# Optimization experiments

Hardware: AMD Instinct MI355X
Metric: run time of the kernel (lower is better)

Reference implementation:

```python
import jax, jax.numpy as jnp
import numpy as np

N_THRESHOLDS = 10


def setup_inputs() -> dict:
    key = jax.random.key(0)
    k1, k2, k3 = jax.random.split(key, 3)
    shape = (32, 1024, 1024)
    prediction = jax.random.normal(k1, shape, dtype=jnp.float32)
    mask = jax.random.randint(k2, shape, 0, 2, dtype=jnp.int32)
    target = jax.random.randint(k3, shape, 0, 2, dtype=jnp.int32)
    return {"prediction": prediction, "mask": mask, "target": target}


def reference(prediction, mask, target):
    # thresholds = linspace(0,1,n+2)[1:-1], same as the torch module
    thresholds = jnp.linspace(0.0, 1.0, N_THRESHOLDS + 2, dtype=jnp.float32)[1:-1]

    s = jax.nn.sigmoid(prediction).ravel()            # [N]
    m = mask.ravel().astype(bool)                     # [N] valid mask
    t = target.ravel().astype(bool)                   # [N]
    mt = m & t                                        # masked positives

    # Broadcast compare against all thresholds at once (single fused pass,
    # no per-threshold host sync like the original loop).
    pos = s[None, :] > thresholds[:, None]            # [T, N] bool

    tp = jnp.sum(pos & mt[None, :], axis=1)           # [T] int32
    p = jnp.sum(pos & m[None, :], axis=1)             # predicted-positive count

    total_m = jnp.sum(m)                              # total valid elements
    total_t = jnp.sum(mt)                             # total true positives in mask

    fp = p - tp
    fn = total_t - tp
    tn = total_m - p - fn

    # classes layout matches torch module: rows = [tp, fp, tn, fn]
    return jnp.stack([tp, fp, tn, fn], axis=0).astype(jnp.float32)
```

## Files before the change

### kernel.cpp

```cpp
#include <hip/hip_runtime.h>


#define NTHR 10
#define NBKT 11
#define NCNT 22
#define WS_STRIDE 16

typedef unsigned long long u64;

__device__ __forceinline__ unsigned wave_reduce_add(unsigned v) {
#pragma unroll
    for (int off = 32; off > 0; off >>= 1)
        v += __shfl_down(v, off, 64);
    return v;
}

__global__ __launch_bounds__(64) void zero_ws_kernel(unsigned* __restrict__ ws) {
    int i = threadIdx.x;
    if (i < NCNT) ws[i * WS_STRIDE] = 0u;
}

__device__ __forceinline__ void acc_elem(float pv, unsigned mm, unsigned tt,
                                         u64& hP, u64& hT) {
    const float L[NTHR] = {-2.3025851f, -1.5040774f, -0.98082925f, -0.55961579f,
                           -0.18232156f, 0.18232156f,  0.55961579f,  0.98082925f,
                            1.5040774f,  2.3025851f};
    unsigned mt = mm & tt;
    unsigned b = 0u;
#pragma unroll
    for (int j = 0; j < NTHR; ++j) b += (pv > L[j]) ? 1u : 0u;
    unsigned sh = (b << 2) + b;
    hP += (u64)mm << sh;
    hT += (u64)mt << sh;
}

__device__ __forceinline__ void acc_vec(const float4& p, const int4& m, const int4& t,
                                        u64& hP, u64& hT) {
    acc_elem(p.x, (unsigned)m.x, (unsigned)t.x, hP, hT);
    acc_elem(p.y, (unsigned)m.y, (unsigned)t.y, hP, hT);
    acc_elem(p.z, (unsigned)m.z, (unsigned)t.z, hP, hT);
    acc_elem(p.w, (unsigned)m.w, (unsigned)t.w, hP, hT);
}

__device__ __forceinline__ void flush_hist(u64& hP, u64& hT,
                                           u64& Plo, u64& Phi, u64& Tlo, u64& Thi) {
#pragma unroll
    for (int b = 0; b < 6; ++b) {
        Plo += (u64)((unsigned)(hP >> (5 * b)) & 31u) << (10 * b);
        Tlo += (u64)((unsigned)(hT >> (5 * b)) & 31u) << (10 * b);
    }
#pragma unroll
    for (int b = 6; b < NBKT; ++b) {
        Phi += (u64)((unsigned)(hP >> (5 * b)) & 31u) << (10 * (b - 6));
        Thi += (u64)((unsigned)(hT >> (5 * b)) & 31u) << (10 * (b - 6));
    }
    hP = 0ull; hT = 0ull;
}

__global__ __launch_bounds__(256, 2) void count_kernel(
        const float4* __restrict__ pred4,
        const int4*  __restrict__ mask4,
        const int4*  __restrict__ targ4,
        const float* __restrict__ pred,
        const int*   __restrict__ mask,
        const int*   __restrict__ targ,
        unsigned* __restrict__ ws, int nvec, int n) {
    u64 Plo = 0ull, Phi = 0ull, Tlo = 0ull, Thi = 0ull;

    const int tid    = blockIdx.x * blockDim.x + threadIdx.x;
    const int lane   = tid & 63;
    const int waveId = tid >> 6;
    const int totalWaves = (gridDim.x * blockDim.x) >> 6;
    const int strideG    = totalWaves << 8;

    float4 cp0, cp1, cp2, cp3;
    int4   cm0, cm1, cm2, cm3, ct0, ct1, ct2, ct3;

    int  base = waveId << 8;
    bool full = (base + 256 <= nvec);
    if (full) {
        cp0 = pred4[base +       lane]; cp1 = pred4[base +  64 + lane];
        cp2 = pred4[base + 128 + lane]; cp3 = pred4[base + 192 + lane];
        cm0 = mask4[base +       lane]; cm1 = mask4[base +  64 + lane];
        cm2 = mask4[base + 128 + lane]; cm3 = mask4[base + 192 + lane];
        ct0 = targ4[base +       lane]; ct1 = targ4[base +  64 + lane];
        ct2 = targ4[base + 128 + lane]; ct3 = targ4[base + 192 + lane];
    }

    while (base < nvec) {
        const int nb    = base + strideG;
        const bool nfull = (nb + 256 <= nvec);

        float4 np0, np1, np2, np3;
        int4   nm0, nm1, nm2, nm3, nt0, nt1, nt2, nt3;
        if (nfull) {
            np0 = pred4[nb +       lane]; np1 = pred4[nb +  64 + lane];
            np2 = pred4[nb + 128 + lane]; np3 = pred4[nb + 192 + lane];
            nm0 = mask4[nb +       lane]; nm1 = mask4[nb +  64 + lane];
            nm2 = mask4[nb + 128 + lane]; nm3 = mask4[nb + 192 + lane];
            nt0 = targ4[nb +       lane]; nt1 = targ4[nb +  64 + lane];
            nt2 = targ4[nb + 128 + lane]; nt3 = targ4[nb + 192 + lane];
        }

        u64 hP = 0ull, hT = 0ull;
        if (full) {
            acc_vec(cp0, cm0, ct0, hP, hT);
            acc_vec(cp1, cm1, ct1, hP, hT);
            acc_vec(cp2, cm2, ct2, hP, hT);
            acc_vec(cp3, cm3, ct3, hP, hT);
        } else {
#pragma unroll
            for (int c = 0; c < 4; ++c) {
                int g = base + (c << 6) + lane;
                if (g < nvec)
                    acc_vec(pred4[g], mask4[g], targ4[g], hP, hT);
            }
        }
        flush_hist(hP, hT, Plo, Phi, Tlo, Thi);

        cp0 = np0; cp1 = np1; cp2 = np2; cp3 = np3;
        cm0 = nm0; cm1 = nm1; cm2 = nm2; cm3 = nm3;
        ct0 = nt0; ct1 = nt1; ct2 = nt2; ct3 = nt3;
        full = nfull;
        base = nb;
    }

    {
        int i = nvec * 4 + tid;
        if (i < n) {
            u64 hP = 0ull, hT = 0ull;
            acc_elem(pred[i], (unsigned)mask[i], (unsigned)targ[i], hP, hT);
            flush_hist(hP, hT, Plo, Phi, Tlo, Thi);
        }
    }

    unsigned vals[NCNT];
#pragma unroll
    for (int b = 0; b < 6; ++b) {
        vals[b]        = (unsigned)(Plo >> (10 * b)) & 1023u;
        vals[NBKT + b] = (unsigned)(Tlo >> (10 * b)) & 1023u;
    }
#pragma unroll
    for (int b = 6; b < NBKT; ++b) {
        vals[b]        = (unsigned)(Phi >> (10 * (b - 6))) & 1023u;
        vals[NBKT + b] = (unsigned)(Thi >> (10 * (b - 6))) & 1023u;
    }
#pragma unroll
    for (int c = 0; c < NCNT; ++c) vals[c] = wave_reduce_add(vals[c]);

    __shared__ unsigned partial[4][NCNT];
    const int wave = threadIdx.x >> 6;
    if ((threadIdx.x & 63) == 0) {
#pragma unroll
        for (int c = 0; c < NCNT; ++c) partial[wave][c] = vals[c];
    }
    __syncthreads();
    if (threadIdx.x < NCNT) {
        unsigned s = partial[0][threadIdx.x] + partial[1][threadIdx.x] +
                     partial[2][threadIdx.x] + partial[3][threadIdx.x];
        atomicAdd(&ws[threadIdx.x * WS_STRIDE], s);
    }
}

__global__ __launch_bounds__(64) void finalize_kernel(const unsigned* __restrict__ ws,
                                                      float* __restrict__ out) {
    int j = threadIdx.x;
    if (j < NTHR) {
        unsigned totM = 0u, totT = 0u, p = 0u, tp = 0u;
#pragma unroll
        for (int b = 0; b < NBKT; ++b) {
            unsigned vP = ws[b * WS_STRIDE];
            unsigned vT = ws[(NBKT + b) * WS_STRIDE];
            totM += vP; totT += vT;
            if (b > j) { p += vP; tp += vT; }
        }
        unsigned fp = p - tp;
        unsigned fn = totT - tp;
        unsigned tn = totM - p - fn;
        out[j]            = (float)tp;
        out[NTHR + j]     = (float)fp;
        out[2 * NTHR + j] = (float)tn;
        out[3 * NTHR + j] = (float)fn;
    }
}

extern "C" void kernel_launch(void* const* d_in, const int* in_sizes, int n_in,
                              void* d_out, int out_size, void* d_ws, size_t ws_size,
                              hipStream_t stream) {
    const float* pred = (const float*)d_in[0];
    const int*   mask = (const int*)d_in[1];
    const int*   targ = (const int*)d_in[2];
    unsigned*    ws   = (unsigned*)d_ws;
    float*       out  = (float*)d_out;

    const int n    = in_sizes[0];
    const int nvec = n / 4;

    zero_ws_kernel<<<1, 64, 0, stream>>>(ws);

    const int blocks = 2048;
    count_kernel<<<blocks, 256, 0, stream>>>(
        (const float4*)pred, (const int4*)mask, (const int4*)targ,
        pred, mask, targ, ws, nvec, n);

    finalize_kernel<<<1, 64, 0, stream>>>(ws, out);
}
```

Measured before the change: 355.5 us.

## Stage inputs through LDS with async global loads and compute buckets via sigmoid

Each wave now streams 64-vector chunks of prediction, mask and target straight into a double-buffered LDS region using global_load_lds, instead of holding a 256-vector register prefetch. The ten threshold compares per element are replaced by a fast sigmoid (expf plus hardware reciprocal) scaled by 11 and truncated to a bucket index. The occupancy hint in launch bounds is dropped. The aim is to free registers and cut ALU work per element. In exchange, fewer bytes are in flight per wave, there is no explicit wait on the async LDS loads before they are read, and the approximate sigmoid may put elements that sit right at a threshold into the wrong bucket.

```diff
diff --git a/kernel.cpp b/kernel.cpp
--- a/kernel.cpp
+++ b/kernel.cpp
@@ -7,6 +7,14 @@
 #define WS_STRIDE 16
 
 typedef unsigned long long u64;
+typedef unsigned u32;
+
+typedef __attribute__((address_space(3))) void* lds_vp;
+typedef const __attribute__((address_space(1))) void* gbl_vp;
+
+__device__ __forceinline__ void ld_lds16(const void* g, void* l) {
+    __builtin_amdgcn_global_load_lds((gbl_vp)g, (lds_vp)l, 16, 0, 0);
+}
 
 __device__ __forceinline__ unsigned wave_reduce_add(unsigned v) {
 #pragma unroll
@@ -15,168 +23,152 @@
     return v;
 }
 
-__global__ __launch_bounds__(64) void zero_ws_kernel(unsigned* __restrict__ ws) {
+__global__ __launch_bounds__(64) void zero_ws_kernel(u32* __restrict__ ws) {
     int i = threadIdx.x;
     if (i < NCNT) ws[i * WS_STRIDE] = 0u;
 }
 
-__device__ __forceinline__ void acc_elem(float pv, unsigned mm, unsigned tt,
-                                         u64& hP, u64& hT) {
-    const float L[NTHR] = {-2.3025851f, -1.5040774f, -0.98082925f, -0.55961579f,
-                           -0.18232156f, 0.18232156f,  0.55961579f,  0.98082925f,
-                            1.5040774f,  2.3025851f};
-    unsigned mt = mm & tt;
-    unsigned b = 0u;
-#pragma unroll
-    for (int j = 0; j < NTHR; ++j) b += (pv > L[j]) ? 1u : 0u;
-    unsigned sh = (b << 2) + b;
+__device__ __forceinline__ void acc_elem(float x, u32 mm, u32 tt, u64& hP, u64& hT) {
+    u32 mt = mm & tt;
+    float e = __expf(-x);
+    float s = __builtin_amdgcn_rcpf(1.0f + e);
+    int bi = (int)(s * 11.0f);
+    u32 b = (u32)(bi > 10 ? 10 : bi);
+    u32 sh = b * 5u;
     hP += (u64)mm << sh;
     hT += (u64)mt << sh;
 }
 
 __device__ __forceinline__ void acc_vec(const float4& p, const int4& m, const int4& t,
                                         u64& hP, u64& hT) {
-    acc_elem(p.x, (unsigned)m.x, (unsigned)t.x, hP, hT);
-    acc_elem(p.y, (unsigned)m.y, (unsigned)t.y, hP, hT);
-    acc_elem(p.z, (unsigned)m.z, (unsigned)t.z, hP, hT);
-    acc_elem(p.w, (unsigned)m.w, (unsigned)t.w, hP, hT);
+    acc_elem(p.x, (u32)m.x, (u32)t.x, hP, hT);
+    acc_elem(p.y, (u32)m.y, (u32)t.y, hP, hT);
+    acc_elem(p.z, (u32)m.z, (u32)t.z, hP, hT);
+    acc_elem(p.w, (u32)m.w, (u32)t.w, hP, hT);
 }
 
 __device__ __forceinline__ void flush_hist(u64& hP, u64& hT,
                                            u64& Plo, u64& Phi, u64& Tlo, u64& Thi) {
 #pragma unroll
     for (int b = 0; b < 6; ++b) {
-        Plo += (u64)((unsigned)(hP >> (5 * b)) & 31u) << (10 * b);
-        Tlo += (u64)((unsigned)(hT >> (5 * b)) & 31u) << (10 * b);
+        Plo += (u64)((u32)(hP >> (5 * b)) & 31u) << (10 * b);
+        Tlo += (u64)((u32)(hT >> (5 * b)) & 31u) << (10 * b);
     }
 #pragma unroll
     for (int b = 6; b < NBKT; ++b) {
-        Phi += (u64)((unsigned)(hP >> (5 * b)) & 31u) << (10 * (b - 6));
-        Thi += (u64)((unsigned)(hT >> (5 * b)) & 31u) << (10 * (b - 6));
+        Phi += (u64)((u32)(hP >> (5 * b)) & 31u) << (10 * (b - 6));
+        Thi += (u64)((u32)(hT >> (5 * b)) & 31u) << (10 * (b - 6));
     }
     hP = 0ull; hT = 0ull;
 }
 
-__global__ __launch_bounds__(256, 2) void count_kernel(
+__global__ __launch_bounds__(256) void count_kernel(
         const float4* __restrict__ pred4,
         const int4*  __restrict__ mask4,
         const int4*  __restrict__ targ4,
         const float* __restrict__ pred,
         const int*   __restrict__ mask,
         const int*   __restrict__ targ,
-        unsigned* __restrict__ ws, int nvec, int n) {
+        u32* __restrict__ ws, int nvec, int n) {
+    __shared__ __align__(16) unsigned char stage[4][2][3][1024];
+    __shared__ u32 partial[4][NCNT];
+
     u64 Plo = 0ull, Phi = 0ull, Tlo = 0ull, Thi = 0ull;
 
-    const int tid    = blockIdx.x * blockDim.x + threadIdx.x;
-    const int lane   = tid & 63;
-    const int waveId = tid >> 6;
+    const int tid        = blockIdx.x * blockDim.x + threadIdx.x;
+    const int lane       = threadIdx.x & 63;
+    const int wv         = threadIdx.x >> 6;
+    const int waveG      = tid >> 6;
     const int totalWaves = (gridDim.x * blockDim.x) >> 6;
-    const int strideG    = totalWaves << 8;
+    const int nchunks    = nvec >> 6;
 
-    float4 cp0, cp1, cp2, cp3;
-    int4   cm0, cm1, cm2, cm3, ct0, ct1, ct2, ct3;
 
-    int  base = waveId << 8;
-    bool full = (base + 256 <= nvec);
-    if (full) {
-        cp0 = pred4[base +       lane]; cp1 = pred4[base +  64 + lane];
-        cp2 = pred4[base + 128 + lane]; cp3 = pred4[base + 192 + lane];
-        cm0 = mask4[base +       lane]; cm1 = mask4[base +  64 + lane];
-        cm2 = mask4[base + 128 + lane]; cm3 = mask4[base + 192 + lane];
-        ct0 = targ4[base +       lane]; ct1 = targ4[base +  64 + lane];
-        ct2 = targ4[base + 128 + lane]; ct3 = targ4[base + 192 + lane];
+    int c   = waveG;
+    int buf = 0;
+    if (c < nchunks) {
+        int gb = c << 6;
+        ld_lds16(pred4 + gb + lane, stage[wv][0][0]);
+        ld_lds16(mask4 + gb + lane, stage[wv][0][1]);
+        ld_lds16(targ4 + gb + lane, stage[wv][0][2]);
+    }
+    while (c < nchunks) {
+        int cn = c + totalWaves;
+        if (cn < nchunks) {
+            int gb = cn << 6;
+            ld_lds16(pred4 + gb + lane, stage[wv][buf ^ 1][0]);
+            ld_lds16(mask4 + gb + lane, stage[wv][buf ^ 1][1]);
+            ld_lds16(targ4 + gb + lane, stage[wv][buf ^ 1][2]);
+        }
+        const float4* lp = (const float4*)stage[wv][buf][0];
+        const int4*   lm = (const int4*)  stage[wv][buf][1];
+        const int4*   lt = (const int4*)  stage[wv][buf][2];
+        float4 p = lp[lane];
+        int4   m = lm[lane];
+        int4   t = lt[lane];
+
+        u64 hP = 0ull, hT = 0ull;
+        acc_vec(p, m, t, hP, hT);
+        flush_hist(hP, hT, Plo, Phi, Tlo, Thi);
+
+        c = cn;
+        buf ^= 1;
     }
 
-    while (base < nvec) {
-        const int nb    = base + strideG;
-        const bool nfull = (nb + 256 <= nvec);
-
-        float4 np0, np1, np2, np3;
-        int4   nm0, nm1, nm2, nm3, nt0, nt1, nt2, nt3;
-        if (nfull) {
-            np0 = pred4[nb +       lane]; np1 = pred4[nb +  64 + lane];
-            np2 = pred4[nb + 128 + lane]; np3 = pred4[nb + 192 + lane];
-            nm0 = mask4[nb +       lane]; nm1 = mask4[nb +  64 + lane];
-            nm2 = mask4[nb + 128 + lane]; nm3 = mask4[nb + 192 + lane];
-            nt0 = targ4[nb +       lane]; nt1 = targ4[nb +  64 + lane];
-            nt2 = targ4[nb + 128 + lane]; nt3 = targ4[nb + 192 + lane];
-        }
-
+    for (int g = (nchunks << 6) + tid; g < nvec; g += gridDim.x * blockDim.x) {
         u64 hP = 0ull, hT = 0ull;
-        if (full) {
-            acc_vec(cp0, cm0, ct0, hP, hT);
-            acc_vec(cp1, cm1, ct1, hP, hT);
-            acc_vec(cp2, cm2, ct2, hP, hT);
-            acc_vec(cp3, cm3, ct3, hP, hT);
-        } else {
-#pragma unroll
-            for (int c = 0; c < 4; ++c) {
-                int g = base + (c << 6) + lane;
-                if (g < nvec)
-                    acc_vec(pred4[g], mask4[g], targ4[g], hP, hT);
-            }
-        }
+        acc_vec(pred4[g], mask4[g], targ4[g], hP, hT);
         flush_hist(hP, hT, Plo, Phi, Tlo, Thi);
-
-        cp0 = np0; cp1 = np1; cp2 = np2; cp3 = np3;
-        cm0 = nm0; cm1 = nm1; cm2 = nm2; cm3 = nm3;
-        ct0 = nt0; ct1 = nt1; ct2 = nt2; ct3 = nt3;
-        full = nfull;
-        base = nb;
     }
-
     {
         int i = nvec * 4 + tid;
         if (i < n) {
             u64 hP = 0ull, hT = 0ull;
-            acc_elem(pred[i], (unsigned)mask[i], (unsigned)targ[i], hP, hT);
+            acc_elem(pred[i], (u32)mask[i], (u32)targ[i], hP, hT);
             flush_hist(hP, hT, Plo, Phi, Tlo, Thi);
         }
     }
 
-    unsigned vals[NCNT];
+    u32 vals[NCNT];
 #pragma unroll
     for (int b = 0; b < 6; ++b) {
-        vals[b]        = (unsigned)(Plo >> (10 * b)) & 1023u;
-        vals[NBKT + b] = (unsigned)(Tlo >> (10 * b)) & 1023u;
+        vals[b]        = (u32)(Plo >> (10 * b)) & 1023u;
+        vals[NBKT + b] = (u32)(Tlo >> (10 * b)) & 1023u;
     }
 #pragma unroll
     for (int b = 6; b < NBKT; ++b) {
-        vals[b]        = (unsigned)(Phi >> (10 * (b - 6))) & 1023u;
-        vals[NBKT + b] = (unsigned)(Thi >> (10 * (b - 6))) & 1023u;
+        vals[b]        = (u32)(Phi >> (10 * (b - 6))) & 1023u;
+        vals[NBKT + b] = (u32)(Thi >> (10 * (b - 6))) & 1023u;
     }
 #pragma unroll
-    for (int c = 0; c < NCNT; ++c) vals[c] = wave_reduce_add(vals[c]);
+    for (int cc = 0; cc < NCNT; ++cc) vals[cc] = wave_reduce_add(vals[cc]);
 
-    __shared__ unsigned partial[4][NCNT];
-    const int wave = threadIdx.x >> 6;
-    if ((threadIdx.x & 63) == 0) {
+    if (lane == 0) {
 #pragma unroll
-        for (int c = 0; c < NCNT; ++c) partial[wave][c] = vals[c];
+        for (int cc = 0; cc < NCNT; ++cc) partial[wv][cc] = vals[cc];
     }
     __syncthreads();
     if (threadIdx.x < NCNT) {
-        unsigned s = partial[0][threadIdx.x] + partial[1][threadIdx.x] +
-                     partial[2][threadIdx.x] + partial[3][threadIdx.x];
+        u32 s = partial[0][threadIdx.x] + partial[1][threadIdx.x] +
+                partial[2][threadIdx.x] + partial[3][threadIdx.x];
         atomicAdd(&ws[threadIdx.x * WS_STRIDE], s);
     }
 }
 
-__global__ __launch_bounds__(64) void finalize_kernel(const unsigned* __restrict__ ws,
+__global__ __launch_bounds__(64) void finalize_kernel(const u32* __restrict__ ws,
                                                       float* __restrict__ out) {
     int j = threadIdx.x;
     if (j < NTHR) {
-        unsigned totM = 0u, totT = 0u, p = 0u, tp = 0u;
+        u32 totM = 0u, totT = 0u, p = 0u, tp = 0u;
 #pragma unroll
         for (int b = 0; b < NBKT; ++b) {
-            unsigned vP = ws[b * WS_STRIDE];
-            unsigned vT = ws[(NBKT + b) * WS_STRIDE];
+            u32 vP = ws[b * WS_STRIDE];
+            u32 vT = ws[(NBKT + b) * WS_STRIDE];
             totM += vP; totT += vT;
             if (b > j) { p += vP; tp += vT; }
         }
-        unsigned fp = p - tp;
-        unsigned fn = totT - tp;
-        unsigned tn = totM - p - fn;
+        u32 fp = p - tp;
+        u32 fn = totT - tp;
+        u32 tn = totM - p - fn;
         out[j]            = (float)tp;
         out[NTHR + j]     = (float)fp;
         out[2 * NTHR + j] = (float)tn;
@@ -190,7 +182,7 @@
     const float* pred = (const float*)d_in[0];
     const int*   mask = (const int*)d_in[1];
     const int*   targ = (const int*)d_in[2];
-    unsigned*    ws   = (unsigned*)d_ws;
+    u32*         ws   = (u32*)d_ws;
     float*       out  = (float*)d_out;
 
     const int n    = in_sizes[0];
```

After: 359.8 us. Within noise of the previous version (+1.2%).
